# Kernel tuning notes

Measured on AMD Instinct MI355X. Metric: run time of the kernel, lower is better.

The kernel has to match this reference:

```python
import jax, jax.numpy as jnp
import numpy as np

TOP_K = 6
CAP_FACTOR = 2.0


def setup_inputs() -> dict:
    key = jax.random.key(0)
    ks = jax.random.split(key, 9)
    B, S, D, F, E, SH = 4, 2048, 512, 256, 64, 2
    return {
        "x": jax.random.normal(ks[0], (B, S, D), jnp.float32),
        "router_w": jax.random.normal(ks[1], (E, D), jnp.float32) * 0.02,
        "bias": jnp.zeros((E,), jnp.float32),
        "shared_w_gate": jax.random.normal(ks[2], (SH, F, D), jnp.float32) * 0.02,
        "shared_w_up": jax.random.normal(ks[3], (SH, F, D), jnp.float32) * 0.02,
        "shared_w_down": jax.random.normal(ks[4], (SH, D, F), jnp.float32) * 0.02,
        "w_gate": jax.random.normal(ks[5], (E, F, D), jnp.float32) * 0.02,
        "w_up": jax.random.normal(ks[6], (E, F, D), jnp.float32) * 0.02,
        "w_down": jax.random.normal(ks[7], (E, D, F), jnp.float32) * 0.02,
    }


def reference(x, router_w, bias, shared_w_gate, shared_w_up, shared_w_down, w_gate, w_up, w_down):
    B, S, D = x.shape
    E = router_w.shape[0]
    K = TOP_K
    N = B * S
    C = max(1, int(N * K * CAP_FACTOR / E))  # static per-expert capacity

    # Router logits with balancing bias (loop_idx=0 row).
    router_logits = jnp.einsum('bsd,ed->bse', x, router_w) + bias

    # Shared experts: averaged SwiGLU over SH experts, fully batched.
    hg = jnp.einsum('bsd,efd->bsef', x, shared_w_gate)
    hu = jnp.einsum('bsd,efd->bsef', x, shared_w_up)
    shared_out = jnp.einsum('bsef,edf->bsd', jax.nn.silu(hg) * hu, shared_w_down)
    shared_out = shared_out / shared_w_gate.shape[0]

    # Top-k routing, renormalised gates.
    router_probs = jax.nn.softmax(router_logits, axis=-1)
    topk_p, topk_i = jax.lax.top_k(router_probs, K)  # [B,S,K]
    topk_p = topk_p / (jnp.sum(topk_p, axis=-1, keepdims=True) + 1e-9)

    x_flat = x.reshape(N, D)
    flat_e = topk_i.reshape(-1)            # [N*K] expert ids
    flat_g = topk_p.reshape(-1)            # [N*K] gates
    token_ids = jnp.repeat(jnp.arange(N), K)

    # Stable sort by expert id -> contiguous expert groups.
    order = jnp.argsort(flat_e)            # jax argsort is stable
    se = flat_e[order]
    st = token_ids[order]
    sg = flat_g[order]

    M = se.shape[0]
    pos = jnp.arange(M)
    is_first = jnp.concatenate([jnp.ones((1,), bool), se[1:] != se[:-1]])
    group_starts = jax.lax.cummax(pos * is_first.astype(pos.dtype))
    slot = pos - group_starts              # position within expert group
    valid = slot < C                       # capacity drop
    safe_slot = jnp.where(valid, slot, C)  # overflow -> scratch slot C

    # Static-shape dispatch buffers (E, C+1, ...); slot C is scratch.
    expert_in = jnp.zeros((E, C + 1, D), x.dtype).at[se, safe_slot].set(x_flat[st])
    expert_gate = jnp.zeros((E, C + 1), x.dtype).at[se, safe_slot].set(sg)
    expert_tok = jnp.full((E, C + 1), N, jnp.int32).at[se, safe_slot].set(st.astype(jnp.int32))
    expert_mask = jnp.zeros((E, C + 1), bool).at[se, safe_slot].set(valid)

    expert_in = expert_in[:, :C]
    expert_gate = expert_gate[:, :C]
    expert_tok = expert_tok[:, :C]
    expert_mask = expert_mask[:, :C]

    # Grouped SwiGLU: three batched GEMMs over experts.
    hg = jnp.einsum('ecd,efd->ecf', expert_in, w_gate)
    hu = jnp.einsum('ecd,efd->ecf', expert_in, w_up)
    expert_out = jnp.einsum('ecf,edf->ecd', jax.nn.silu(hg) * hu, w_down)

    # Combine: scatter-add gated outputs back to tokens; row N is a sink.
    fm = expert_mask.reshape(-1)
    dst = jnp.where(fm, expert_tok.reshape(-1), N)
    fg = jnp.where(fm, expert_gate.reshape(-1), jnp.zeros((), x.dtype))
    sparse = jax.ops.segment_sum(fg[:, None] * expert_out.reshape(-1, D), dst, num_segments=N + 1)[:N]

    return shared_out + sparse.reshape(B, S, D)
```

## Files before the change

kernel.cpp:

```cpp
#include <hip/hip_runtime.h>
#include <hip/hip_bf16.h>
#include <math.h>

#define N_TOK 8192
#define D_DIM 512
#define F_DIM 256
#define E_NUM 64
#define SH_NUM 2
#define K_TOP 6
#define CAP   1536
#define M_ENT (N_TOK * K_TOP)
#define NCHUNK (M_ENT / 256)

#define EW_STRIDE 393216
#define E_TOT (E_NUM + SH_NUM)
#define X_BF_BYTES   (8388608ull)
#define WT_BYTES     ((size_t)E_TOT * EW_STRIDE * 2)
#define TOK_ROUTED   (E_NUM * CAP)
#define TOK_TOTAL    (TOK_ROUTED + SH_NUM * N_TOK)
#define EO_BYTES     ((size_t)TOK_TOTAL * D_DIM * 2)
#define RWT_BYTES    131072ull

#define SLOT 18432

typedef __attribute__((ext_vector_type(8))) short bf16x8;
typedef __attribute__((ext_vector_type(8))) short short8;
typedef __attribute__((ext_vector_type(4))) float f32x4;

#define VMCNT(n) asm volatile("s_waitcnt vmcnt(" #n ")" ::: "memory")

__device__ __forceinline__ ushort f2bf(float f) {
  union { float f; unsigned u; } c; c.f = f;
  return (ushort)((c.u + 0x7FFFu + ((c.u >> 16) & 1u)) >> 16);
}
__device__ __forceinline__ float bf2f(ushort h) {
  union { unsigned u; float f; } c; c.u = ((unsigned)h) << 16;
  return c.f;
}
__device__ __forceinline__ void gload16(const void* g, void* l) {
  __builtin_amdgcn_global_load_lds(
      (const __attribute__((address_space(1))) void*)g,
      (__attribute__((address_space(3))) void*)l, 16, 0, 0);
}

__global__ void router_topk(const float* __restrict__ x, const float* __restrict__ rw,
                            const float* __restrict__ bias, int* __restrict__ topk_i,
                            float* __restrict__ topk_p) {
  const int wave = threadIdx.x >> 6;
  const int lane = threadIdx.x & 63;
  const int n = blockIdx.x * 4 + wave;
  if (n >= N_TOK) return;

  const float4* xr = (const float4*)(x + (size_t)n * D_DIM);
  const float4* wr = (const float4*)(rw + (size_t)lane * D_DIM);
  float acc = 0.f;
  #pragma unroll 4
  for (int d4 = 0; d4 < D_DIM / 4; ++d4) {
    float4 xv = xr[d4]; float4 wv = wr[d4];
    acc += xv.x * wv.x + xv.y * wv.y + xv.z * wv.z + xv.w * wv.w;
  }
  float logit = acc + bias[lane];

  float m = logit;
  for (int off = 32; off > 0; off >>= 1) m = fmaxf(m, __shfl_xor(m, off));
  float p = expf(logit - m);
  float s = p;
  for (int off = 32; off > 0; off >>= 1) s += __shfl_xor(s, off);
  float prob = p / s;

  float myp = prob;
  float gsum = 0.f;
  float myg = 0.f; int myi = -1;
  for (int k = 0; k < K_TOP; ++k) {
    float bp = myp; int bi = lane;
    for (int off = 32; off > 0; off >>= 1) {
      float op = __shfl_xor(bp, off); int oi = __shfl_xor(bi, off);
      if (op > bp || (op == bp && oi < bi)) { bp = op; bi = oi; }
    }
    gsum += bp;
    if (lane == k) { myg = bp; myi = bi; }
    if (lane == bi) myp = -1.f;
  }
  if (lane < K_TOP) {
    topk_i[n * K_TOP + lane] = myi;
    topk_p[n * K_TOP + lane] = myg / (gsum + 1e-9f);
  }
}

__global__ void transpose_rw(const float* __restrict__ rw, float* __restrict__ rwt) {
  int idx = blockIdx.x * 256 + threadIdx.x;
  if (idx >= E_NUM * (D_DIM / 4)) return;
  int e = idx >> 7, k4 = idx & 127;
  float4 v = *(const float4*)(rw + (size_t)e * D_DIM + k4 * 4);
  *(float4*)(rwt + ((size_t)k4 * 64 + e) * 4) = v;
}

__device__ __forceinline__ void softmax_topk_write(float logit, int n, int lane,
                                                   int* __restrict__ topk_i,
                                                   float* __restrict__ topk_p) {
  float m = logit;
  for (int off = 32; off > 0; off >>= 1) m = fmaxf(m, __shfl_xor(m, off));
  float p = expf(logit - m);
  float s = p;
  for (int off = 32; off > 0; off >>= 1) s += __shfl_xor(s, off);
  float prob = p / s;

  float myp = prob;
  float gsum = 0.f;
  float myg = 0.f; int myi = -1;
  #pragma unroll 1
  for (int k = 0; k < K_TOP; ++k) {
    float bp = myp; int bi = lane;
    for (int off = 32; off > 0; off >>= 1) {
      float op = __shfl_xor(bp, off); int oi = __shfl_xor(bi, off);
      if (op > bp || (op == bp && oi < bi)) { bp = op; bi = oi; }
    }
    gsum += bp;
    if (lane == k) { myg = bp; myi = bi; }
    if (lane == bi) myp = -1.f;
  }
  if (lane < K_TOP) {
    topk_i[n * K_TOP + lane] = myi;
    topk_p[n * K_TOP + lane] = myg / (gsum + 1e-9f);
  }
}

__global__ void __launch_bounds__(256) router_topk2(
    const float* __restrict__ x, const float* __restrict__ rwt,
    const float* __restrict__ bias, int* __restrict__ topk_i,
    float* __restrict__ topk_p) {
  const int wave = threadIdx.x >> 6;
  const int lane = threadIdx.x & 63;
  const int n0 = blockIdx.x * 32 + wave * 8;

  float acc[8];
  #pragma unroll
  for (int t = 0; t < 8; ++t) acc[t] = 0.f;

  const float4* wv4 = (const float4*)rwt;
  #pragma unroll 2
  for (int k4 = 0; k4 < 128; ++k4) {
    float4 w = wv4[k4 * 64 + lane];
    #pragma unroll
    for (int t = 0; t < 8; ++t) {
      float4 xv = *(const float4*)(x + (size_t)(n0 + t) * D_DIM + k4 * 4);
      acc[t] += xv.x * w.x + xv.y * w.y + xv.z * w.z + xv.w * w.w;
    }
  }
  float b = bias[lane];
  #pragma unroll 1
  for (int t = 0; t < 8; ++t)
    softmax_topk_write(acc[t] + b, n0 + t, lane, topk_i, topk_p);
}

__global__ void hist_kernel(const int* __restrict__ topk_i, int* __restrict__ chunk_hist) {
  __shared__ int h[E_NUM];
  const int tid = threadIdx.x;
  if (tid < E_NUM) h[tid] = 0;
  __syncthreads();
  int e = topk_i[blockIdx.x * 256 + tid];
  atomicAdd(&h[e], 1);
  __syncthreads();
  if (tid < E_NUM) chunk_hist[blockIdx.x * E_NUM + tid] = h[tid];
}

__global__ void scan_kernel(const int* __restrict__ chunk_hist, int* __restrict__ chunk_base) {
  const int e = threadIdx.x;
  int run = 0;
  for (int c = 0; c < NCHUNK; ++c) {
    chunk_base[c * E_NUM + e] = run;
    run += chunk_hist[c * E_NUM + e];
  }
}

__global__ void dispatch_kernel(const int* __restrict__ topk_i, const float* __restrict__ topk_p,
                                const int* __restrict__ chunk_base,
                                int* __restrict__ expert_tok, float* __restrict__ expert_gate,
                                int* __restrict__ entry_row) {
  __shared__ int eid[256];
  const int tid = threadIdx.x;
  const int m = blockIdx.x * 256 + tid;
  const int e = topk_i[m];
  eid[tid] = e;
  __syncthreads();
  int rank = 0;
  for (int t = 0; t < tid; ++t) rank += (eid[t] == e);
  int slot = chunk_base[blockIdx.x * E_NUM + e] + rank;
  int row = -1;
  if (slot < CAP) {
    expert_tok[e * CAP + slot] = m / K_TOP;
    expert_gate[e * CAP + slot] = topk_p[m];
    row = e * CAP + slot;
  }
  if (entry_row) entry_row[m] = row;
}


__global__ void convert_x(const float* __restrict__ x, ushort* __restrict__ xb) {
  size_t idx = (size_t)blockIdx.x * 256 + threadIdx.x;
  const float4* s4 = (const float4*)(x + idx * 8);
  float4 v0 = s4[0], v1 = s4[1];
  short8 o;
  o[0] = f2bf(v0.x); o[1] = f2bf(v0.y); o[2] = f2bf(v0.z); o[3] = f2bf(v0.w);
  o[4] = f2bf(v1.x); o[5] = f2bf(v1.y); o[6] = f2bf(v1.z); o[7] = f2bf(v1.w);
  *(short8*)(xb + idx * 8) = o;
}

__global__ void convert_w(const float* __restrict__ wg_, const float* __restrict__ wu_,
                          const float* __restrict__ wd_, const float* __restrict__ swg,
                          const float* __restrict__ swu, const float* __restrict__ swd,
                          ushort* __restrict__ Wt) {
  int e = blockIdx.x / 12;
  int rem = blockIdx.x - e * 12;
  int p = rem >> 2, q = rem & 3;
  const float* src;
  if (p == 0)      src = (e < E_NUM) ? wg_ + (size_t)e * 131072 : swg + (size_t)(e - E_NUM) * 131072;
  else if (p == 1) src = (e < E_NUM) ? wu_ + (size_t)e * 131072 : swu + (size_t)(e - E_NUM) * 131072;
  else             src = (e < E_NUM) ? wd_ + (size_t)e * 131072 : swd + (size_t)(e - E_NUM) * 131072;
  ushort* dst = Wt + (size_t)e * EW_STRIDE + (size_t)p * 131072;
  #pragma unroll
  for (int i = 0; i < 16; ++i) {
    int d = q * 32768 + i * 2048 + threadIdx.x * 8;
    int ci = d >> 13;
    int r  = d & 8191;
    int nt = r >> 9;
    int rr = r & 511;
    int k8 = rr >> 7;
    int n  = nt * 16 + ((rr >> 3) & 15);
    size_t srcidx;
    if (p < 2) {
      srcidx = (size_t)n * 512 + ci * 32 + k8 * 8;
    } else {
      int np = ci >> 3, kc = ci & 7;
      srcidx = (size_t)(np * 256 + n) * 256 + kc * 32 + k8 * 8;
    }
    const float4* s4 = (const float4*)(src + srcidx);
    float4 v0 = s4[0], v1 = s4[1];
    short8 o;
    o[0] = f2bf(v0.x); o[1] = f2bf(v0.y); o[2] = f2bf(v0.z); o[3] = f2bf(v0.w);
    o[4] = f2bf(v1.x); o[5] = f2bf(v1.y); o[6] = f2bf(v1.z); o[7] = f2bf(v1.w);
    *(short8*)(dst + d) = o;
  }
}

__global__ void init_shared_tok(int* __restrict__ tok_all, float* __restrict__ gate_all) {
  int i = blockIdx.x * 256 + threadIdx.x;
  tok_all[TOK_ROUTED + i] = i & (N_TOK - 1);
  gate_all[TOK_ROUTED + i] = 0.5f;
}

template <bool GATHER>
__global__ void __launch_bounds__(512, 1) ffn_mfma(
    const ushort* __restrict__ xb, const ushort* __restrict__ Wt,
    const int* __restrict__ tok_all, const float* __restrict__ gate_all,
    float* __restrict__ out, ushort* __restrict__ expert_out) {
  int e, tbase;
  {
    int xcd = blockIdx.x & 7;
    int j = blockIdx.x >> 3;
    if (j < 192) {
      int ec = j / 24;
      int mt = j - ec * 24;
      e = ec * 8 + xcd;
      tbase = e * CAP + mt * 64;
      if (tok_all[tbase] < 0) return;
    } else {
      int s = xcd * 32 + (j - 192);
      int sh = s & 1, mt = s >> 1;
      e = E_NUM + sh;
      tbase = TOK_ROUTED + sh * N_TOK + mt * 64;
    }
  }
  const ushort* wbase = Wt + (size_t)e * EW_STRIDE;

  __shared__ ushort RING[3 * SLOT];
  __shared__ ushort Act[16384];
  __shared__ int   toks[64];
  __shared__ float gts[64];

  const int tid = threadIdx.x;
  const int lane = tid & 63;
  const int wid = tid >> 6;
  const int wr = wid >> 2;
  const int wc = wid & 3;
  const int rl = lane & 15;
  const int hi = lane >> 4;

  if (tid < 64) {
    int t = tok_all[tbase + tid];
    toks[tid] = t;
    gts[tid] = (t >= 0) ? gate_all[tbase + tid] : 0.f;
  }
  __syncthreads();

  int stok = 0;
  if (wid < 4) { int t = toks[wid * 16 + rl]; stok = (t < 0) ? 0 : t; }
  const ushort* xsrc = xb + (size_t)stok * D_DIM + hi * 8;

  auto stage_gu = [&](int sl, int kc) {
    ushort* dst = RING + sl * SLOT;
    if (wid < 4)
      gload16(xsrc + kc * 32, dst + wid * 512);
    #pragma unroll
    for (int i = 0; i < 2; ++i) {
      int s = wid * 2 + i;
      gload16(wbase + kc * 8192 + s * 512 + lane * 8, dst + 2048 + s * 512);
      gload16(wbase + 131072 + kc * 8192 + s * 512 + lane * 8, dst + 10240 + s * 512);
    }
  };
  auto stage_dn = [&](int sl, int kc) {
    ushort* dst = RING + sl * SLOT;
    #pragma unroll
    for (int i = 0; i < 4; ++i) {
      int s = wid * 4 + i;
      gload16(wbase + 262144 + (s >> 4) * 65536 + kc * 8192 + (s & 15) * 512 + lane * 8,
              dst + s * 512);
    }
  };

  const f32x4 fzero = {0.f, 0.f, 0.f, 0.f};
  f32x4 accg[2][4], accu[2][4];
  #pragma unroll
  for (int ri = 0; ri < 2; ++ri)
    #pragma unroll
    for (int bi = 0; bi < 4; ++bi) { accg[ri][bi] = fzero; accu[ri][bi] = fzero; }

  stage_gu(0, 0); stage_gu(1, 1);
  {
    int sl_c = 0, sl_n = 2;
    #pragma unroll 1
    for (int kc = 0; kc < 16; ++kc) {
      if (kc < 14) { stage_gu(sl_n, kc + 2); sl_n = (sl_n == 2) ? 0 : sl_n + 1; }
      if (kc < 14)      { if (wid < 4) VMCNT(10); else VMCNT(8); }
      else if (kc == 14){ if (wid < 4) VMCNT(5);  else VMCNT(4); }
      else              VMCNT(0);
      __builtin_amdgcn_s_barrier();
      __builtin_amdgcn_sched_barrier(0);
      {
        const ushort* base = RING + sl_c * SLOT;
        bf16x8 a[2], bg[4], bu[4];
        #pragma unroll
        for (int ri = 0; ri < 2; ++ri)
          a[ri] = *(const bf16x8*)(base + (wr * 2 + ri) * 512 + lane * 8);
        #pragma unroll
        for (int bi = 0; bi < 4; ++bi) {
          bg[bi] = *(const bf16x8*)(base + 2048 + (wc * 4 + bi) * 512 + lane * 8);
          bu[bi] = *(const bf16x8*)(base + 10240 + (wc * 4 + bi) * 512 + lane * 8);
        }
        __builtin_amdgcn_s_setprio(1);
        #pragma unroll
        for (int ri = 0; ri < 2; ++ri)
          #pragma unroll
          for (int bi = 0; bi < 4; ++bi) {
            accg[ri][bi] = __builtin_amdgcn_mfma_f32_16x16x32_bf16(a[ri], bg[bi], accg[ri][bi], 0, 0, 0);
            accu[ri][bi] = __builtin_amdgcn_mfma_f32_16x16x32_bf16(a[ri], bu[bi], accu[ri][bi], 0, 0, 0);
          }
        __builtin_amdgcn_s_setprio(0);
      }
      sl_c = (sl_c == 2) ? 0 : sl_c + 1;
      __builtin_amdgcn_s_barrier();
    }
  }

  #pragma unroll
  for (int ri = 0; ri < 2; ++ri)
    #pragma unroll
    for (int bi = 0; bi < 4; ++bi) {
      int st = (wr * 2 + ri) * 8 + wc * 2 + (bi >> 1);
      int base = st * 512 + ((bi & 1) * 2 + (rl >> 3)) * 128 + (rl & 7);
      #pragma unroll
      for (int j = 0; j < 4; ++j) {
        float g = accg[ri][bi][j], u = accu[ri][bi][j];
        Act[base + (hi * 4 + j) * 8] = f2bf(g / (1.f + __expf(-g)) * u);
      }
    }

  f32x4 accd[2][8];
  #pragma unroll
  for (int ri = 0; ri < 2; ++ri)
    #pragma unroll
    for (int bj = 0; bj < 8; ++bj) accd[ri][bj] = fzero;

  stage_dn(0, 0); stage_dn(1, 1);
  asm volatile("s_waitcnt lgkmcnt(0)" ::: "memory");
  __builtin_amdgcn_s_barrier();
  __builtin_amdgcn_sched_barrier(0);
  {
    int sl_c = 0, sl_n = 2;
    #pragma unroll 1
    for (int kc = 0; kc < 8; ++kc) {
      if (kc < 6) { stage_dn(sl_n, kc + 2); sl_n = (sl_n == 2) ? 0 : sl_n + 1; }
      if (kc < 6)       VMCNT(8);
      else if (kc == 6) VMCNT(4);
      else              VMCNT(0);
      __builtin_amdgcn_s_barrier();
      __builtin_amdgcn_sched_barrier(0);
      {
        const ushort* base = RING + sl_c * SLOT;
        bf16x8 a[2], b[8];
        #pragma unroll
        for (int ri = 0; ri < 2; ++ri)
          a[ri] = *(const bf16x8*)(Act + ((wr * 2 + ri) * 8 + kc) * 512 + lane * 8);
        #pragma unroll
        for (int bj = 0; bj < 8; ++bj)
          b[bj] = *(const bf16x8*)(base + (wc * 8 + bj) * 512 + lane * 8);
        __builtin_amdgcn_s_setprio(1);
        #pragma unroll
        for (int ri = 0; ri < 2; ++ri)
          #pragma unroll
          for (int bj = 0; bj < 8; ++bj)
            accd[ri][bj] = __builtin_amdgcn_mfma_f32_16x16x32_bf16(a[ri], b[bj], accd[ri][bj], 0, 0, 0);
        __builtin_amdgcn_s_setprio(0);
      }
      sl_c = (sl_c == 2) ? 0 : sl_c + 1;
      __builtin_amdgcn_s_barrier();
    }
  }

  if (GATHER) {
    #pragma unroll
    for (int ri = 0; ri < 2; ++ri)
      #pragma unroll
      for (int j = 0; j < 4; ++j) {
        int r = wr * 32 + ri * 16 + hi * 4 + j;
        if (toks[r] < 0) continue;
        ushort* erow = expert_out + (size_t)(tbase + r) * D_DIM + wc * 128 + rl;
        #pragma unroll
        for (int bj = 0; bj < 8; ++bj)
          erow[bj * 16] = f2bf(accd[ri][bj][j]);
      }
  } else {
    #pragma unroll
    for (int ri = 0; ri < 2; ++ri)
      #pragma unroll
      for (int j = 0; j < 4; ++j) {
        int r = wr * 32 + ri * 16 + hi * 4 + j;
        int t = toks[r];
        if (t < 0) continue;
        float gt = gts[r];
        float* orow = out + (size_t)t * D_DIM + wc * 128 + rl;
        #pragma unroll
        for (int bj = 0; bj < 8; ++bj)
          atomicAdd(orow + bj * 16, gt * accd[ri][bj][j]);
      }
  }
}

__global__ void __launch_bounds__(256) gather_out(
    const ushort* __restrict__ eo, const int* __restrict__ entry_row,
    const float* __restrict__ topk_p, float* __restrict__ out) {
  const int t = blockIdx.x * 4 + (threadIdx.x >> 6);
  const int lane = threadIdx.x & 63;
  const int base = t * K_TOP;

  float acc[8];
  #pragma unroll
  for (int j = 0; j < 8; ++j) acc[j] = 0.f;

  #pragma unroll
  for (int k = 0; k < K_TOP; ++k) {
    int row = entry_row[base + k];
    if (row >= 0) {
      float g = topk_p[base + k];
      bf16x8 v = *(const bf16x8*)(eo + (size_t)row * D_DIM + lane * 8);
      #pragma unroll
      for (int j = 0; j < 8; ++j) acc[j] += g * bf2f((ushort)v[j]);
    }
  }
  #pragma unroll
  for (int sh = 0; sh < SH_NUM; ++sh) {
    int row = TOK_ROUTED + sh * N_TOK + t;
    bf16x8 v = *(const bf16x8*)(eo + (size_t)row * D_DIM + lane * 8);
    #pragma unroll
    for (int j = 0; j < 8; ++j) acc[j] += 0.5f * bf2f((ushort)v[j]);
  }
  float4* o = (float4*)(out + (size_t)t * D_DIM + lane * 8);
  o[0] = make_float4(acc[0], acc[1], acc[2], acc[3]);
  o[1] = make_float4(acc[4], acc[5], acc[6], acc[7]);
}


__global__ void __launch_bounds__(256, 2) expert_ffn_mfma(
    const float* __restrict__ x, const float* __restrict__ wg_,
    const float* __restrict__ wu_, const float* __restrict__ wd_,
    const int* __restrict__ expert_tok, const float* __restrict__ expert_gate,
    float* __restrict__ out) {
  const int e = blockIdx.x & (E_NUM - 1);
  const int mt = blockIdx.x >> 6;
  const int s0 = mt * 64;
  if (expert_tok[e * CAP + s0] < 0) return;

  __shared__ ushort Xs[64][72];
  __shared__ ushort Ws[256][72];
  __shared__ ushort Act[64][264];
  __shared__ int   toks[64];
  __shared__ float gts[64];

  const int tid = threadIdx.x;
  const int lane = tid & 63;
  const int wid = tid >> 6;
  const int rl = lane & 15;
  const int ko = (lane >> 4) * 8;
  const int rquad = (lane >> 4) * 4;

  if (tid < 64) {
    int t = expert_tok[e * CAP + s0 + tid];
    toks[tid] = t;
    gts[tid] = (t >= 0) ? expert_gate[e * CAP + s0 + tid] : 0.f;
  }
  __syncthreads();

  float4 px[4], pw[16];

  auto loadX = [&](int kb) {
    #pragma unroll
    for (int it = 0; it < 4; ++it) {
      int idx = tid + it * 256;
      int row = idx >> 4, c4 = (idx & 15) << 2;
      int t = toks[row];
      px[it] = (t >= 0) ? *(const float4*)(x + (size_t)t * D_DIM + kb * 64 + c4)
                        : make_float4(0.f, 0.f, 0.f, 0.f);
    }
  };
  auto writeX = [&]() {
    #pragma unroll
    for (int it = 0; it < 4; ++it) {
      int idx = tid + it * 256;
      int row = idx >> 4, c4 = (idx & 15) << 2;
      ushort4 h; h.x = f2bf(px[it].x); h.y = f2bf(px[it].y);
      h.z = f2bf(px[it].z); h.w = f2bf(px[it].w);
      *(ushort4*)&Xs[row][c4] = h;
    }
  };
  auto loadW = [&](const float* src, int ldk, int kb) {
    #pragma unroll
    for (int it = 0; it < 16; ++it) {
      int idx = tid + it * 256;
      int row = idx >> 4, c4 = (idx & 15) << 2;
      pw[it] = *(const float4*)(src + (size_t)row * ldk + kb * 64 + c4);
    }
  };
  auto writeW = [&]() {
    #pragma unroll
    for (int it = 0; it < 16; ++it) {
      int idx = tid + it * 256;
      int row = idx >> 4, c4 = (idx & 15) << 2;
      ushort4 h; h.x = f2bf(pw[it].x); h.y = f2bf(pw[it].y);
      h.z = f2bf(pw[it].z); h.w = f2bf(pw[it].w);
      *(ushort4*)&Ws[row][c4] = h;
    }
  };
  auto compute = [&](const ushort* Ab, int lda, f32x4 (&acc)[4][4]) {
    #pragma unroll
    for (int kk = 0; kk < 2; ++kk) {
      bf16x8 a[4], b[4];
      #pragma unroll
      for (int ri = 0; ri < 4; ++ri)
        a[ri] = *(const bf16x8*)(Ab + (size_t)(ri * 16 + rl) * lda + kk * 32 + ko);
      #pragma unroll
      for (int bi = 0; bi < 4; ++bi)
        b[bi] = *(const bf16x8*)(&Ws[wid * 64 + bi * 16 + rl][kk * 32 + ko]);
      #pragma unroll
      for (int ri = 0; ri < 4; ++ri)
        #pragma unroll
        for (int bi = 0; bi < 4; ++bi)
          acc[ri][bi] = __builtin_amdgcn_mfma_f32_16x16x32_bf16(a[ri], b[bi], acc[ri][bi], 0, 0, 0);
    }
  };

  const f32x4 fzero = {0.f, 0.f, 0.f, 0.f};

  #pragma unroll 1
  for (int which = 0; which < 2; ++which) {
    const float* wsrc = (which == 0 ? wg_ : wu_) + (size_t)e * F_DIM * D_DIM;
    f32x4 acc[4][4];
    #pragma unroll
    for (int ri = 0; ri < 4; ++ri)
      #pragma unroll
      for (int bi = 0; bi < 4; ++bi) acc[ri][bi] = fzero;

    loadX(0); loadW(wsrc, D_DIM, 0);
    writeX(); writeW();
    __syncthreads();
    for (int kb = 0; kb < 8; ++kb) {
      if (kb < 7) { loadX(kb + 1); loadW(wsrc, D_DIM, kb + 1); }
      compute(&Xs[0][0], 72, acc);
      __syncthreads();
      if (kb < 7) { writeX(); writeW(); __syncthreads(); }
    }
    #pragma unroll
    for (int ri = 0; ri < 4; ++ri)
      #pragma unroll
      for (int bi = 0; bi < 4; ++bi)
        #pragma unroll
        for (int j = 0; j < 4; ++j) {
          int r = ri * 16 + rquad + j;
          int c = wid * 64 + bi * 16 + rl;
          if (which == 0) {
            Act[r][c] = f2bf(acc[ri][bi][j]);
          } else {
            float hg = bf2f(Act[r][c]);
            float a = hg / (1.f + __expf(-hg)) * acc[ri][bi][j];
            Act[r][c] = f2bf(a);
          }
        }
    __syncthreads();
  }

  #pragma unroll 1
  for (int np = 0; np < 2; ++np) {
    const float* wsrc = wd_ + ((size_t)e * D_DIM + np * 256) * F_DIM;
    f32x4 acc[4][4];
    #pragma unroll
    for (int ri = 0; ri < 4; ++ri)
      #pragma unroll
      for (int bi = 0; bi < 4; ++bi) acc[ri][bi] = fzero;

    loadW(wsrc, F_DIM, 0); writeW();
    __syncthreads();
    for (int kb = 0; kb < 4; ++kb) {
      if (kb < 3) loadW(wsrc, F_DIM, kb + 1);
      compute(&Act[0][kb * 64], 264, acc);
      __syncthreads();
      if (kb < 3) { writeW(); __syncthreads(); }
    }
    #pragma unroll
    for (int ri = 0; ri < 4; ++ri)
      #pragma unroll
      for (int bi = 0; bi < 4; ++bi)
        #pragma unroll
        for (int j = 0; j < 4; ++j) {
          int r = ri * 16 + rquad + j;
          int t = toks[r];
          if (t >= 0) {
            int c = np * 256 + wid * 64 + bi * 16 + rl;
            atomicAdd(out + (size_t)t * D_DIM + c, gts[r] * acc[ri][bi][j]);
          }
        }
  }
}

__global__ void __launch_bounds__(256, 2) shared_ffn_mfma(
    const float* __restrict__ x, const float* __restrict__ swg,
    const float* __restrict__ swu, const float* __restrict__ swd,
    float* __restrict__ out) {
  const int row0 = blockIdx.x * 32;

  __shared__ ushort Xs[32][72];
  __shared__ ushort Ws[256][72];
  __shared__ ushort Act[32][264];

  const int tid = threadIdx.x;
  const int lane = tid & 63;
  const int wid = tid >> 6;
  const int rl = lane & 15;
  const int ko = (lane >> 4) * 8;
  const int rquad = (lane >> 4) * 4;

  float4 px[2], pw[16];

  auto loadX = [&](int kb) {
    #pragma unroll
    for (int it = 0; it < 2; ++it) {
      int idx = tid + it * 256;
      int row = idx >> 4, c4 = (idx & 15) << 2;
      px[it] = *(const float4*)(x + (size_t)(row0 + row) * D_DIM + kb * 64 + c4);
    }
  };
  auto writeX = [&]() {
    #pragma unroll
    for (int it = 0; it < 2; ++it) {
      int idx = tid + it * 256;
      int row = idx >> 4, c4 = (idx & 15) << 2;
      ushort4 h; h.x = f2bf(px[it].x); h.y = f2bf(px[it].y);
      h.z = f2bf(px[it].z); h.w = f2bf(px[it].w);
      *(ushort4*)&Xs[row][c4] = h;
    }
  };
  auto loadW = [&](const float* src, int ldk, int kb) {
    #pragma unroll
    for (int it = 0; it < 16; ++it) {
      int idx = tid + it * 256;
      int row = idx >> 4, c4 = (idx & 15) << 2;
      pw[it] = *(const float4*)(src + (size_t)row * ldk + kb * 64 + c4);
    }
  };
  auto writeW = [&]() {
    #pragma unroll
    for (int it = 0; it < 16; ++it) {
      int idx = tid + it * 256;
      int row = idx >> 4, c4 = (idx & 15) << 2;
      ushort4 h; h.x = f2bf(pw[it].x); h.y = f2bf(pw[it].y);
      h.z = f2bf(pw[it].z); h.w = f2bf(pw[it].w);
      *(ushort4*)&Ws[row][c4] = h;
    }
  };
  auto compute = [&](const ushort* Ab, int lda, f32x4 (&acc)[2][4]) {
    #pragma unroll
    for (int kk = 0; kk < 2; ++kk) {
      bf16x8 a[2], b[4];
      #pragma unroll
      for (int ri = 0; ri < 2; ++ri)
        a[ri] = *(const bf16x8*)(Ab + (size_t)(ri * 16 + rl) * lda + kk * 32 + ko);
      #pragma unroll
      for (int bi = 0; bi < 4; ++bi)
        b[bi] = *(const bf16x8*)(&Ws[wid * 64 + bi * 16 + rl][kk * 32 + ko]);
      #pragma unroll
      for (int ri = 0; ri < 2; ++ri)
        #pragma unroll
        for (int bi = 0; bi < 4; ++bi)
          acc[ri][bi] = __builtin_amdgcn_mfma_f32_16x16x32_bf16(a[ri], b[bi], acc[ri][bi], 0, 0, 0);
    }
  };

  const f32x4 fzero = {0.f, 0.f, 0.f, 0.f};
  f32x4 accd[2][2][4];
  #pragma unroll
  for (int np = 0; np < 2; ++np)
    #pragma unroll
    for (int ri = 0; ri < 2; ++ri)
      #pragma unroll
      for (int bi = 0; bi < 4; ++bi) accd[np][ri][bi] = fzero;

  #pragma unroll 1
  for (int sh = 0; sh < SH_NUM; ++sh) {
    #pragma unroll 1
    for (int which = 0; which < 2; ++which) {
      const float* wsrc = (which == 0 ? swg : swu) + (size_t)sh * F_DIM * D_DIM;
      f32x4 acc[2][4];
      #pragma unroll
      for (int ri = 0; ri < 2; ++ri)
        #pragma unroll
        for (int bi = 0; bi < 4; ++bi) acc[ri][bi] = fzero;

      loadX(0); loadW(wsrc, D_DIM, 0);
      writeX(); writeW();
      __syncthreads();
      for (int kb = 0; kb < 8; ++kb) {
        if (kb < 7) { loadX(kb + 1); loadW(wsrc, D_DIM, kb + 1); }
        compute(&Xs[0][0], 72, acc);
        __syncthreads();
        if (kb < 7) { writeX(); writeW(); __syncthreads(); }
      }
      #pragma unroll
      for (int ri = 0; ri < 2; ++ri)
        #pragma unroll
        for (int bi = 0; bi < 4; ++bi)
          #pragma unroll
          for (int j = 0; j < 4; ++j) {
            int r = ri * 16 + rquad + j;
            int c = wid * 64 + bi * 16 + rl;
            if (which == 0) {
              Act[r][c] = f2bf(acc[ri][bi][j]);
            } else {
              float hg = bf2f(Act[r][c]);
              float a = hg / (1.f + __expf(-hg)) * acc[ri][bi][j];
              Act[r][c] = f2bf(a);
            }
          }
      __syncthreads();
    }
    #pragma unroll
    for (int np = 0; np < 2; ++np) {
      const float* wsrc = swd + ((size_t)sh * D_DIM + np * 256) * F_DIM;
      loadW(wsrc, F_DIM, 0); writeW();
      __syncthreads();
      for (int kb = 0; kb < 4; ++kb) {
        if (kb < 3) loadW(wsrc, F_DIM, kb + 1);
        compute(&Act[0][kb * 64], 264, accd[np]);
        __syncthreads();
        if (kb < 3) { writeW(); __syncthreads(); }
      }
    }
  }

  #pragma unroll
  for (int np = 0; np < 2; ++np)
    #pragma unroll
    for (int ri = 0; ri < 2; ++ri)
      #pragma unroll
      for (int bi = 0; bi < 4; ++bi)
        #pragma unroll
        for (int j = 0; j < 4; ++j) {
          int r = ri * 16 + rquad + j;
          int c = np * 256 + wid * 64 + bi * 16 + rl;
          out[(size_t)(row0 + r) * D_DIM + c] = 0.5f * accd[np][ri][bi][j];
        }
}

extern "C" void kernel_launch(void* const* d_in, const int* in_sizes, int n_in,
                              void* d_out, int out_size, void* d_ws, size_t ws_size,
                              hipStream_t stream) {
  const float* x    = (const float*)d_in[0];
  const float* rw   = (const float*)d_in[1];
  const float* bias = (const float*)d_in[2];
  const float* swg  = (const float*)d_in[3];
  const float* swu  = (const float*)d_in[4];
  const float* swd  = (const float*)d_in[5];
  const float* wg   = (const float*)d_in[6];
  const float* wu   = (const float*)d_in[7];
  const float* wd   = (const float*)d_in[8];
  float* out = (float*)d_out;

  const size_t small = 2 * (size_t)M_ENT * 4 + (size_t)M_ENT * 4 +
                       2 * (size_t)NCHUNK * E_NUM * 4 + 2 * (size_t)TOK_TOTAL * 4 +
                       RWT_BYTES;
  const size_t need_mid = X_BF_BYTES + WT_BYTES + small;
  const size_t need_big = need_mid + EO_BYTES;

  if (ws_size >= need_mid) {
    const bool gather = (ws_size >= need_big);
    char* ws = (char*)d_ws;
    ushort* x_bf     = (ushort*)ws; ws += X_BF_BYTES;
    ushort* Wt       = (ushort*)ws; ws += WT_BYTES;
    int*   topk_i    = (int*)ws;    ws += (size_t)M_ENT * 4;
    float* topk_p    = (float*)ws;  ws += (size_t)M_ENT * 4;
    int*   entry_row = (int*)ws;    ws += (size_t)M_ENT * 4;
    int*   chunk_hist= (int*)ws;    ws += (size_t)NCHUNK * E_NUM * 4;
    int*   chunk_base= (int*)ws;    ws += (size_t)NCHUNK * E_NUM * 4;
    int*   tok_all   = (int*)ws;    ws += (size_t)TOK_TOTAL * 4;
    float* gate_all  = (float*)ws;  ws += (size_t)TOK_TOTAL * 4;
    float* rwt       = (float*)ws;  ws += RWT_BYTES;
    ushort* eo       = (ushort*)ws;

    transpose_rw<<<32, 256, 0, stream>>>(rw, rwt);
    convert_x<<<2048, 256, 0, stream>>>(x, x_bf);
    convert_w<<<E_TOT * 12, 256, 0, stream>>>(wg, wu, wd, swg, swu, swd, Wt);
    router_topk2<<<256, 256, 0, stream>>>(x, rwt, bias, topk_i, topk_p);
    hipMemsetAsync(tok_all, 0xFF, (size_t)TOK_ROUTED * 4, stream);
    if (!gather) hipMemsetAsync(out, 0, (size_t)out_size * 4, stream);
    hist_kernel<<<NCHUNK, 256, 0, stream>>>(topk_i, chunk_hist);
    scan_kernel<<<1, 64, 0, stream>>>(chunk_hist, chunk_base);
    dispatch_kernel<<<NCHUNK, 256, 0, stream>>>(topk_i, topk_p, chunk_base, tok_all,
                                                gate_all, entry_row);
    init_shared_tok<<<64, 256, 0, stream>>>(tok_all, gate_all);
    const int nblk = 2 * (N_TOK / 64) + (CAP / 64) * E_NUM;
    if (gather) {
      ffn_mfma<true><<<nblk, 512, 0, stream>>>(x_bf, Wt, tok_all, gate_all, out, eo);
      gather_out<<<N_TOK / 4, 256, 0, stream>>>(eo, entry_row, topk_p, out);
    } else {
      ffn_mfma<false><<<nblk, 512, 0, stream>>>(x_bf, Wt, tok_all, gate_all, out, nullptr);
    }
  } else {
    char* ws = (char*)d_ws;
    int*   topk_i      = (int*)ws;   ws += (size_t)M_ENT * 4;
    float* topk_p      = (float*)ws; ws += (size_t)M_ENT * 4;
    int*   chunk_hist  = (int*)ws;   ws += (size_t)NCHUNK * E_NUM * 4;
    int*   chunk_base  = (int*)ws;   ws += (size_t)NCHUNK * E_NUM * 4;
    int*   expert_tok  = (int*)ws;   ws += (size_t)E_NUM * CAP * 4;
    float* expert_gate = (float*)ws; ws += (size_t)E_NUM * CAP * 4;

    router_topk<<<N_TOK / 4, 256, 0, stream>>>(x, rw, bias, topk_i, topk_p);
    hipMemsetAsync(expert_tok, 0xFF, (size_t)E_NUM * CAP * 4, stream);
    hist_kernel<<<NCHUNK, 256, 0, stream>>>(topk_i, chunk_hist);
    scan_kernel<<<1, 64, 0, stream>>>(chunk_hist, chunk_base);
    dispatch_kernel<<<NCHUNK, 256, 0, stream>>>(topk_i, topk_p, chunk_base, expert_tok,
                                                expert_gate, nullptr);
    shared_ffn_mfma<<<N_TOK / 32, 256, 0, stream>>>(x, swg, swu, swd, out);
    expert_ffn_mfma<<<(CAP / 64) * E_NUM, 256, 0, stream>>>(x, wg, wu, wd, expert_tok,
                                                            expert_gate, out);
  }
}
```

Measured before the change: 283.8 us.

## Double FFN token tile to 128 rows with double-buffered ring; fuse prep kernels

```diff
diff --git a/kernel.cpp b/kernel.cpp
--- a/kernel.cpp
+++ b/kernel.cpp
@@ -21,7 +21,7 @@
 #define EO_BYTES     ((size_t)TOK_TOTAL * D_DIM * 2)
 #define RWT_BYTES    131072ull
 
-#define SLOT 18432
+#define SLOT 20480
 
 typedef __attribute__((ext_vector_type(8))) short bf16x8;
 typedef __attribute__((ext_vector_type(8))) short short8;
@@ -85,14 +85,6 @@
     topk_i[n * K_TOP + lane] = myi;
     topk_p[n * K_TOP + lane] = myg / (gsum + 1e-9f);
   }
-}
-
-__global__ void transpose_rw(const float* __restrict__ rw, float* __restrict__ rwt) {
-  int idx = blockIdx.x * 256 + threadIdx.x;
-  if (idx >= E_NUM * (D_DIM / 4)) return;
-  int e = idx >> 7, k4 = idx & 127;
-  float4 v = *(const float4*)(rw + (size_t)e * D_DIM + k4 * 4);
-  *(float4*)(rwt + ((size_t)k4 * 64 + e) * 4) = v;
 }
 
 __device__ __forceinline__ void softmax_topk_write(float logit, int n, int lane,
@@ -196,14 +188,28 @@
 }
 
 
-__global__ void convert_x(const float* __restrict__ x, ushort* __restrict__ xb) {
-  size_t idx = (size_t)blockIdx.x * 256 + threadIdx.x;
-  const float4* s4 = (const float4*)(x + idx * 8);
-  float4 v0 = s4[0], v1 = s4[1];
-  short8 o;
-  o[0] = f2bf(v0.x); o[1] = f2bf(v0.y); o[2] = f2bf(v0.z); o[3] = f2bf(v0.w);
-  o[4] = f2bf(v1.x); o[5] = f2bf(v1.y); o[6] = f2bf(v1.z); o[7] = f2bf(v1.w);
-  *(short8*)(xb + idx * 8) = o;
+__global__ void convert_x_misc(const float* __restrict__ x, ushort* __restrict__ xb,
+                               const float* __restrict__ rw, float* __restrict__ rwt,
+                               int* __restrict__ tok_all, float* __restrict__ gate_all) {
+  int b = blockIdx.x;
+  if (b < 2048) {
+    size_t idx = (size_t)b * 256 + threadIdx.x;
+    const float4* s4 = (const float4*)(x + idx * 8);
+    float4 v0 = s4[0], v1 = s4[1];
+    short8 o;
+    o[0] = f2bf(v0.x); o[1] = f2bf(v0.y); o[2] = f2bf(v0.z); o[3] = f2bf(v0.w);
+    o[4] = f2bf(v1.x); o[5] = f2bf(v1.y); o[6] = f2bf(v1.z); o[7] = f2bf(v1.w);
+    *(short8*)(xb + idx * 8) = o;
+  } else if (b < 2080) {
+    int idx = (b - 2048) * 256 + threadIdx.x;
+    int e = idx >> 7, k4 = idx & 127;
+    float4 v = *(const float4*)(rw + (size_t)e * D_DIM + k4 * 4);
+    *(float4*)(rwt + ((size_t)k4 * 64 + e) * 4) = v;
+  } else {
+    int i = (b - 2080) * 256 + threadIdx.x;
+    tok_all[TOK_ROUTED + i] = i & (N_TOK - 1);
+    gate_all[TOK_ROUTED + i] = 0.5f;
+  }
 }
 
 __global__ void convert_w(const float* __restrict__ wg_, const float* __restrict__ wu_,
@@ -243,12 +249,6 @@
   }
 }
 
-__global__ void init_shared_tok(int* __restrict__ tok_all, float* __restrict__ gate_all) {
-  int i = blockIdx.x * 256 + threadIdx.x;
-  tok_all[TOK_ROUTED + i] = i & (N_TOK - 1);
-  gate_all[TOK_ROUTED + i] = 0.5f;
-}
-
 template <bool GATHER>
 __global__ void __launch_bounds__(512, 1) ffn_mfma(
     const ushort* __restrict__ xb, const ushort* __restrict__ Wt,
@@ -258,25 +258,25 @@
   {
     int xcd = blockIdx.x & 7;
     int j = blockIdx.x >> 3;
-    if (j < 192) {
-      int ec = j / 24;
-      int mt = j - ec * 24;
+    if (j < 96) {
+      int ec = j / 12;
+      int mt = j - ec * 12;
       e = ec * 8 + xcd;
-      tbase = e * CAP + mt * 64;
+      tbase = e * CAP + mt * 128;
       if (tok_all[tbase] < 0) return;
     } else {
-      int s = xcd * 32 + (j - 192);
+      int s = xcd * 16 + (j - 96);
       int sh = s & 1, mt = s >> 1;
       e = E_NUM + sh;
-      tbase = TOK_ROUTED + sh * N_TOK + mt * 64;
+      tbase = TOK_ROUTED + sh * N_TOK + mt * 128;
     }
   }
   const ushort* wbase = Wt + (size_t)e * EW_STRIDE;
 
-  __shared__ ushort RING[3 * SLOT];
-  __shared__ ushort Act[16384];
-  __shared__ int   toks[64];
-  __shared__ float gts[64];
+  __shared__ ushort RING[2 * SLOT];
+  __shared__ ushort Act[32768];
+  __shared__ int   toks[128];
+  __shared__ float gts[128];
 
   const int tid = threadIdx.x;
   const int lane = tid & 63;
@@ -286,26 +286,24 @@
   const int rl = lane & 15;
   const int hi = lane >> 4;
 
-  if (tid < 64) {
+  if (tid < 128) {
     int t = tok_all[tbase + tid];
     toks[tid] = t;
     gts[tid] = (t >= 0) ? gate_all[tbase + tid] : 0.f;
   }
   __syncthreads();
 
-  int stok = 0;
-  if (wid < 4) { int t = toks[wid * 16 + rl]; stok = (t < 0) ? 0 : t; }
-  const ushort* xsrc = xb + (size_t)stok * D_DIM + hi * 8;
+  int t0 = toks[wid * 16 + rl];
+  const ushort* xsrc = xb + (size_t)(t0 < 0 ? 0 : t0) * D_DIM + hi * 8;
 
   auto stage_gu = [&](int sl, int kc) {
     ushort* dst = RING + sl * SLOT;
-    if (wid < 4)
-      gload16(xsrc + kc * 32, dst + wid * 512);
+    gload16(xsrc + kc * 32, dst + wid * 512);
     #pragma unroll
     for (int i = 0; i < 2; ++i) {
       int s = wid * 2 + i;
-      gload16(wbase + kc * 8192 + s * 512 + lane * 8, dst + 2048 + s * 512);
-      gload16(wbase + 131072 + kc * 8192 + s * 512 + lane * 8, dst + 10240 + s * 512);
+      gload16(wbase + kc * 8192 + s * 512 + lane * 8, dst + 4096 + s * 512);
+      gload16(wbase + 131072 + kc * 8192 + s * 512 + lane * 8, dst + 12288 + s * 512);
     }
   };
   auto stage_dn = [&](int sl, int kc) {
@@ -319,54 +317,50 @@
   };
 
   const f32x4 fzero = {0.f, 0.f, 0.f, 0.f};
-  f32x4 accg[2][4], accu[2][4];
-  #pragma unroll
-  for (int ri = 0; ri < 2; ++ri)
+  f32x4 accg[4][4], accu[4][4];
+  #pragma unroll
+  for (int ri = 0; ri < 4; ++ri)
     #pragma unroll
     for (int bi = 0; bi < 4; ++bi) { accg[ri][bi] = fzero; accu[ri][bi] = fzero; }
 
-  stage_gu(0, 0); stage_gu(1, 1);
+  stage_gu(0, 0);
   {
-    int sl_c = 0, sl_n = 2;
+    int sl = 0;
     #pragma unroll 1
     for (int kc = 0; kc < 16; ++kc) {
-      if (kc < 14) { stage_gu(sl_n, kc + 2); sl_n = (sl_n == 2) ? 0 : sl_n + 1; }
-      if (kc < 14)      { if (wid < 4) VMCNT(10); else VMCNT(8); }
-      else if (kc == 14){ if (wid < 4) VMCNT(5);  else VMCNT(4); }
-      else              VMCNT(0);
+      if (kc < 15) { stage_gu(sl ^ 1, kc + 1); VMCNT(5); }
+      else         VMCNT(0);
       __builtin_amdgcn_s_barrier();
       __builtin_amdgcn_sched_barrier(0);
       {
-        const ushort* base = RING + sl_c * SLOT;
-        bf16x8 a[2], bg[4], bu[4];
-        #pragma unroll
-        for (int ri = 0; ri < 2; ++ri)
-          a[ri] = *(const bf16x8*)(base + (wr * 2 + ri) * 512 + lane * 8);
+        const ushort* base = RING + sl * SLOT;
+        bf16x8 a[4];
+        #pragma unroll
+        for (int ri = 0; ri < 4; ++ri)
+          a[ri] = *(const bf16x8*)(base + (wr * 4 + ri) * 512 + lane * 8);
+        __builtin_amdgcn_s_setprio(1);
         #pragma unroll
         for (int bi = 0; bi < 4; ++bi) {
-          bg[bi] = *(const bf16x8*)(base + 2048 + (wc * 4 + bi) * 512 + lane * 8);
-          bu[bi] = *(const bf16x8*)(base + 10240 + (wc * 4 + bi) * 512 + lane * 8);
+          bf16x8 bg = *(const bf16x8*)(base + 4096 + (wc * 4 + bi) * 512 + lane * 8);
+          bf16x8 bu = *(const bf16x8*)(base + 12288 + (wc * 4 + bi) * 512 + lane * 8);
+          #pragma unroll
+          for (int ri = 0; ri < 4; ++ri) {
+            accg[ri][bi] = __builtin_amdgcn_mfma_f32_16x16x32_bf16(a[ri], bg, accg[ri][bi], 0, 0, 0);
+            accu[ri][bi] = __builtin_amdgcn_mfma_f32_16x16x32_bf16(a[ri], bu, accu[ri][bi], 0, 0, 0);
+          }
         }
-        __builtin_amdgcn_s_setprio(1);
-        #pragma unroll
-        for (int ri = 0; ri < 2; ++ri)
-          #pragma unroll
-          for (int bi = 0; bi < 4; ++bi) {
-            accg[ri][bi] = __builtin_amdgcn_mfma_f32_16x16x32_bf16(a[ri], bg[bi], accg[ri][bi], 0, 0, 0);
-            accu[ri][bi] = __builtin_amdgcn_mfma_f32_16x16x32_bf16(a[ri], bu[bi], accu[ri][bi], 0, 0, 0);
-          }
         __builtin_amdgcn_s_setprio(0);
       }
-      sl_c = (sl_c == 2) ? 0 : sl_c + 1;
+      sl ^= 1;
       __builtin_amdgcn_s_barrier();
     }
   }
 
   #pragma unroll
-  for (int ri = 0; ri < 2; ++ri)
+  for (int ri = 0; ri < 4; ++ri)
     #pragma unroll
     for (int bi = 0; bi < 4; ++bi) {
-      int st = (wr * 2 + ri) * 8 + wc * 2 + (bi >> 1);
+      int st = (wr * 4 + ri) * 8 + wc * 2 + (bi >> 1);
       int base = st * 512 + ((bi & 1) * 2 + (rl >> 3)) * 128 + (rl & 7);
       #pragma unroll
       for (int j = 0; j < 4; ++j) {
@@ -374,55 +368,50 @@
         Act[base + (hi * 4 + j) * 8] = f2bf(g / (1.f + __expf(-g)) * u);
       }
     }
-
-  f32x4 accd[2][8];
-  #pragma unroll
-  for (int ri = 0; ri < 2; ++ri)
+  stage_dn(0, 0);
+  __syncthreads();
+
+  f32x4 accd[4][8];
+  #pragma unroll
+  for (int ri = 0; ri < 4; ++ri)
     #pragma unroll
     for (int bj = 0; bj < 8; ++bj) accd[ri][bj] = fzero;
 
-  stage_dn(0, 0); stage_dn(1, 1);
-  asm volatile("s_waitcnt lgkmcnt(0)" ::: "memory");
-  __builtin_amdgcn_s_barrier();
-  __builtin_amdgcn_sched_barrier(0);
   {
-    int sl_c = 0, sl_n = 2;
+    int sl = 0;
     #pragma unroll 1
     for (int kc = 0; kc < 8; ++kc) {
-      if (kc < 6) { stage_dn(sl_n, kc + 2); sl_n = (sl_n == 2) ? 0 : sl_n + 1; }
-      if (kc < 6)       VMCNT(8);
-      else if (kc == 6) VMCNT(4);
-      else              VMCNT(0);
+      if (kc < 7) { stage_dn(sl ^ 1, kc + 1); VMCNT(4); }
+      else        VMCNT(0);
       __builtin_amdgcn_s_barrier();
       __builtin_amdgcn_sched_barrier(0);
       {
-        const ushort* base = RING + sl_c * SLOT;
-        bf16x8 a[2], b[8];
-        #pragma unroll
-        for (int ri = 0; ri < 2; ++ri)
-          a[ri] = *(const bf16x8*)(Act + ((wr * 2 + ri) * 8 + kc) * 512 + lane * 8);
-        #pragma unroll
-        for (int bj = 0; bj < 8; ++bj)
-          b[bj] = *(const bf16x8*)(base + (wc * 8 + bj) * 512 + lane * 8);
+        const ushort* base = RING + sl * SLOT;
+        bf16x8 a[4];
+        #pragma unroll
+        for (int ri = 0; ri < 4; ++ri)
+          a[ri] = *(const bf16x8*)(Act + ((wr * 4 + ri) * 8 + kc) * 512 + lane * 8);
         __builtin_amdgcn_s_setprio(1);
         #pragma unroll
-        for (int ri = 0; ri < 2; ++ri)
+        for (int bj = 0; bj < 8; ++bj) {
+          bf16x8 b = *(const bf16x8*)(base + (wc >> 1) * 8192 + ((wc & 1) * 8 + bj) * 512 + lane * 8);
           #pragma unroll
-          for (int bj = 0; bj < 8; ++bj)
-            accd[ri][bj] = __builtin_amdgcn_mfma_f32_16x16x32_bf16(a[ri], b[bj], accd[ri][bj], 0, 0, 0);
+          for (int ri = 0; ri < 4; ++ri)
+            accd[ri][bj] = __builtin_amdgcn_mfma_f32_16x16x32_bf16(a[ri], b, accd[ri][bj], 0, 0, 0);
+        }
         __builtin_amdgcn_s_setprio(0);
       }
-      sl_c = (sl_c == 2) ? 0 : sl_c + 1;
+      sl ^= 1;
       __builtin_amdgcn_s_barrier();
     }
   }
 
   if (GATHER) {
     #pragma unroll
-    for (int ri = 0; ri < 2; ++ri)
+    for (int ri = 0; ri < 4; ++ri)
       #pragma unroll
       for (int j = 0; j < 4; ++j) {
-        int r = wr * 32 + ri * 16 + hi * 4 + j;
+        int r = wr * 64 + ri * 16 + hi * 4 + j;
         if (toks[r] < 0) continue;
         ushort* erow = expert_out + (size_t)(tbase + r) * D_DIM + wc * 128 + rl;
         #pragma unroll
@@ -431,10 +420,10 @@
       }
   } else {
     #pragma unroll
-    for (int ri = 0; ri < 2; ++ri)
+    for (int ri = 0; ri < 4; ++ri)
       #pragma unroll
       for (int j = 0; j < 4; ++j) {
-        int r = wr * 32 + ri * 16 + hi * 4 + j;
+        int r = wr * 64 + ri * 16 + hi * 4 + j;
         int t = toks[r];
         if (t < 0) continue;
         float gt = gts[r];
@@ -823,8 +812,7 @@
     float* rwt       = (float*)ws;  ws += RWT_BYTES;
     ushort* eo       = (ushort*)ws;
 
-    transpose_rw<<<32, 256, 0, stream>>>(rw, rwt);
-    convert_x<<<2048, 256, 0, stream>>>(x, x_bf);
+    convert_x_misc<<<2144, 256, 0, stream>>>(x, x_bf, rw, rwt, tok_all, gate_all);
     convert_w<<<E_TOT * 12, 256, 0, stream>>>(wg, wu, wd, swg, swu, swd, Wt);
     router_topk2<<<256, 256, 0, stream>>>(x, rwt, bias, topk_i, topk_p);
     hipMemsetAsync(tok_all, 0xFF, (size_t)TOK_ROUTED * 4, stream);
@@ -833,8 +821,7 @@
     scan_kernel<<<1, 64, 0, stream>>>(chunk_hist, chunk_base);
     dispatch_kernel<<<NCHUNK, 256, 0, stream>>>(topk_i, topk_p, chunk_base, tok_all,
                                                 gate_all, entry_row);
-    init_shared_tok<<<64, 256, 0, stream>>>(tok_all, gate_all);
-    const int nblk = 2 * (N_TOK / 64) + (CAP / 64) * E_NUM;
+    const int nblk = (CAP / 128) * E_NUM + 2 * (N_TOK / 128);
     if (gather) {
       ffn_mfma<true><<<nblk, 512, 0, stream>>>(x_bf, Wt, tok_all, gate_all, out, eo);
       gather_out<<<N_TOK / 4, 256, 0, stream>>>(eo, entry_row, topk_p, out);
```

After: 262.1 us. 1.08x faster.
